# Optimization experiments

Hardware: AMD Instinct MI355X
Metric: run time of the kernel (lower is better)

## Reference

```python
import jax, jax.numpy as jnp
import numpy as np

D_MODEL = 1024
D_STATE = 16
EXPAND = 2
D_CONV = 4
D_INNER = EXPAND * D_MODEL
BATCH = 1
SEQLEN = 2048


def setup_inputs() -> dict:
    key = jax.random.key(0)
    ks = jax.random.split(key, 8)
    s = 0.02
    x = jax.random.normal(ks[0], (BATCH, SEQLEN, D_MODEL), jnp.float32)
    W_in = jax.random.normal(ks[1], (2 * D_INNER, D_MODEL), jnp.float32) * s
    conv_w = jax.random.normal(ks[2], (D_INNER, 1, D_CONV), jnp.float32) * s
    conv_b = jnp.zeros((D_INNER,), jnp.float32)
    # A_log init as in module: log(arange(1, d_state+1)) tiled over d_inner
    A_log = jnp.log(jnp.tile(jnp.arange(1, D_STATE + 1, dtype=jnp.float32), (D_INNER, 1)))
    D_param = jnp.ones((D_INNER,), jnp.float32)
    W_x = jax.random.normal(ks[3], (2 * D_STATE, D_INNER), jnp.float32) * s
    W_dt = jax.random.normal(ks[4], (D_INNER, D_INNER), jnp.float32) * s
    b_dt = jnp.zeros((D_INNER,), jnp.float32)
    W_out = jax.random.normal(ks[5], (D_MODEL, D_INNER), jnp.float32) * s
    return {"x": x, "W_in": W_in, "conv_w": conv_w, "conv_b": conv_b,
            "A_log": A_log, "D_param": D_param, "W_x": W_x,
            "W_dt": W_dt, "b_dt": b_dt, "W_out": W_out}


def reference(x, W_in, conv_w, conv_b, A_log, D_param, W_x, W_dt, b_dt, W_out):
    B_, L, _ = x.shape
    xz = jnp.einsum('bld,ed->ble', x, W_in)          # [B,L,2*d_inner]
    x_inner, z = jnp.split(xz, 2, axis=-1)
    # causal depthwise conv1d (pad left d_conv-1 == torch pad-both + slice[:L])
    xc = jax.lax.conv_general_dilated(
        jnp.swapaxes(x_inner, 1, 2), conv_w, (1,), [(D_CONV - 1, 0)],
        feature_group_count=D_INNER,
        dimension_numbers=('NCH', 'OIH', 'NCH')) + conv_b[None, :, None]
    x_ssm = jnp.swapaxes(jax.nn.silu(xc), 1, 2)       # [B,L,d_inner]
    dt = jax.nn.softplus(jnp.einsum('ble,fe->blf', x_ssm, W_dt) + b_dt)
    x_dbl = jnp.einsum('ble,se->bls', x_ssm, W_x)     # [B,L,2*d_state]
    B_mat, C_mat = jnp.split(x_dbl, 2, axis=-1)       # each [B,L,d_state]
    A = -jnp.exp(A_log)                               # [d_inner,d_state]
    dA = jnp.exp(dt[..., None] * A)                   # [B,L,d_inner,d_state]
    dBx = B_mat[:, :, None, :] * dt[..., None] * x_ssm[..., None]

    def step(h, inp):
        dA_t, dBx_t, C_t = inp
        h = dA_t * h + dBx_t                          # [B,d_inner,d_state]
        y_t = jnp.einsum('bds,bs->bd', h, C_t)
        return h, y_t

    h0 = jnp.zeros((B_, D_INNER, D_STATE), x.dtype)
    _, ys = jax.lax.scan(step, h0, (jnp.swapaxes(dA, 0, 1),
                                    jnp.swapaxes(dBx, 0, 1),
                                    jnp.swapaxes(C_mat, 0, 1)))
    y = jnp.swapaxes(ys, 0, 1) + D_param * x_ssm      # [B,L,d_inner]
    y = y * jax.nn.silu(z)
    out = jnp.einsum('ble,de->bld', y, W_out)
    return out + x
```

## Files before the change

kernel.cpp:

```cpp
#include <hip/hip_runtime.h>

#define L_SEQ 2048
#define DMODEL 1024
#define DINNER 2048
#define NCHUNK 128
#define TCHUNK 16

typedef __attribute__((ext_vector_type(8))) short bf16x8;
typedef __attribute__((ext_vector_type(4))) float f32x4;

__device__ __forceinline__ float bf2f(unsigned short u) {
  return __uint_as_float(((unsigned)u) << 16);
}
__device__ __forceinline__ unsigned short f2bf(float f) {
  unsigned u = __float_as_uint(f);
  return (unsigned short)((u + 0x7FFFu + ((u >> 16) & 1u)) >> 16);
}
__device__ __forceinline__ void gload_lds16(const void* g, void* l) {
  __builtin_amdgcn_global_load_lds(
      (const __attribute__((address_space(1))) void*)g,
      (__attribute__((address_space(3))) void*)l, 16, 0, 0);
}

__global__ void cvt_f32_bf16(const float4* __restrict__ in, ushort4* __restrict__ out, int n4) {
  int i = blockIdx.x * blockDim.x + threadIdx.x;
  if (i >= n4) return;
  float4 v = in[i];
  ushort4 o;
  o.x = f2bf(v.x); o.y = f2bf(v.y); o.z = f2bf(v.z); o.w = f2bf(v.w);
  out[i] = o;
}

__global__ void zero_bf16(ushort4* __restrict__ out, int n4) {
  int i = blockIdx.x * blockDim.x + threadIdx.x;
  if (i >= n4) return;
  out[i] = ushort4{0, 0, 0, 0};
}

template <int EPI>
__global__ __launch_bounds__(256) void gemm_bt3(
    const unsigned short* __restrict__ A, const unsigned short* __restrict__ B,
    int M, int N, int K, int nx, int ksplit,
    float* __restrict__ outf, unsigned short* __restrict__ outb,
    const float* __restrict__ aux) {
  __shared__ __align__(16) unsigned short As[3 * 128 * 32];
  __shared__ __align__(16) unsigned short Bs[3 * 128 * 32];
  const int tid = threadIdx.x;
  const int lane = tid & 63;
  const int wave = tid >> 6;
  const int wm = wave >> 1, wn = wave & 1;

  const int nwg = gridDim.x;
  const int wg = blockIdx.x;
  const int swzb = (wg & 7) * (nwg >> 3) + (wg >> 3);
  const int tiles = nwg / ksplit;
  const int ks = swzb / tiles;
  const int t = swzb - ks * tiles;
  const int bx = t % nx, by = t / nx;
  const int bm = by * 128, bn = bx * 128;
  const int Ks = K / ksplit;
  const int kbeg = ks * Ks;
  const int nk = Ks >> 5;

  const int srow = tid >> 2, sc4 = tid & 3;
  const int scp = sc4 ^ ((srow >> 1) & 3);
  const unsigned short* Ag = A + (size_t)(bm + srow) * K + scp * 8;
  const unsigned short* Bg = B + (size_t)(bn + srow) * K + scp * 8;
  unsigned short* AsW = &As[srow * 32 + sc4 * 8];
  unsigned short* BsW = &Bs[srow * 32 + sc4 * 8];

  auto STAGE = [&](int buf, int k0) {
    gload_lds16(Ag + k0, AsW + buf * 4096);
    gload_lds16(Ag + (size_t)64 * K + k0, AsW + buf * 4096 + 64 * 32);
    gload_lds16(Bg + k0, BsW + buf * 4096);
    gload_lds16(Bg + (size_t)64 * K + k0, BsW + buf * 4096 + 64 * 32);
  };

  f32x4 acc[4][4] = {};

  const int g = lane >> 4;
  const int r16 = lane & 15;
  const int sw = (g ^ ((r16 >> 1) & 3)) * 8;

  STAGE(0, kbeg);
  STAGE(1, kbeg + 32);
  int cur = 0, stg = 2;

  for (int i = 0; i < nk; ++i) {
    if (i < nk - 1) {
      asm volatile("s_waitcnt vmcnt(4)" ::: "memory");
    } else {
      asm volatile("s_waitcnt vmcnt(0)" ::: "memory");
    }
    __builtin_amdgcn_s_barrier();
    asm volatile("" ::: "memory");
    if (i + 2 < nk) {
      STAGE(stg, kbeg + (i + 2) * 32);
      stg = (stg == 2) ? 0 : stg + 1;
    }

    bf16x8 a[4], b[4];
#pragma unroll
    for (int ii = 0; ii < 4; ++ii)
      a[ii] = *(const bf16x8*)&As[cur * 4096 + (wm * 64 + ii * 16 + r16) * 32 + sw];
#pragma unroll
    for (int j = 0; j < 4; ++j)
      b[j] = *(const bf16x8*)&Bs[cur * 4096 + (wn * 64 + j * 16 + r16) * 32 + sw];
#pragma unroll
    for (int ii = 0; ii < 4; ++ii)
#pragma unroll
      for (int j = 0; j < 4; ++j)
        acc[ii][j] = __builtin_amdgcn_mfma_f32_16x16x32_bf16(a[ii], b[j], acc[ii][j], 0, 0, 0);

    cur = (cur == 2) ? 0 : cur + 1;
  }

  const int rq = lane >> 4;
#pragma unroll
  for (int i = 0; i < 4; ++i)
#pragma unroll
    for (int j = 0; j < 4; ++j)
#pragma unroll
      for (int r = 0; r < 4; ++r) {
        int row = bm + wm * 64 + i * 16 + rq * 4 + r;
        int col = bn + wn * 64 + j * 16 + r16;
        float v = acc[i][j][r];
        if (EPI == 0) {
          outb[(size_t)row * N + col] = f2bf(v);
        } else if (EPI == 3) {
          if (col < 2048) {
            float tt = v + aux[col];
            float sp = (tt > 15.f) ? tt : log1pf(__expf(tt));
            outb[(size_t)row * 2048 + col] = f2bf(sp);
          } else if (col < 2080) {
            outf[(size_t)row * 32 + (col - 2048)] = v;
          }
        } else {
          outf[(size_t)ks * M * N + (size_t)row * N + col] = v;
        }
      }
}

__global__ void reduce_addx(const float4* __restrict__ p, const float4* __restrict__ x,
                            float4* __restrict__ out, int n4) {
  int i = blockIdx.x * 256 + threadIdx.x;
  if (i >= n4) return;
  float4 a = p[i], b = p[n4 + i], c = x[i];
  float4 o;
  o.x = a.x + b.x + c.x; o.y = a.y + b.y + c.y;
  o.z = a.z + b.z + c.z; o.w = a.w + b.w + c.w;
  out[i] = o;
}

__global__ __launch_bounds__(256) void conv_silu8(
    const unsigned short* __restrict__ xz,
    const float* __restrict__ cw, const float* __restrict__ cb,
    unsigned short* __restrict__ x_ssm, unsigned short* __restrict__ sz_out) {
  int idx = blockIdx.x * 256 + threadIdx.x;
  int l = idx >> 8, c0 = (idx & 255) * 8;
  float acc[8];
  float4 b0 = *(const float4*)(cb + c0);
  float4 b1 = *(const float4*)(cb + c0 + 4);
  acc[0] = b0.x; acc[1] = b0.y; acc[2] = b0.z; acc[3] = b0.w;
  acc[4] = b1.x; acc[5] = b1.y; acc[6] = b1.z; acc[7] = b1.w;
  float4 w[8];
#pragma unroll
  for (int j = 0; j < 8; ++j) w[j] = *(const float4*)(cw + (c0 + j) * 4);
#pragma unroll
  for (int k = 0; k < 4; ++k) {
    int lt = l - 3 + k;
    if (lt >= 0) {
      bf16x8 v = *(const bf16x8*)(xz + (size_t)lt * 4096 + c0);
      const float* wk = (const float*)w;
#pragma unroll
      for (int j = 0; j < 8; ++j)
        acc[j] = fmaf(bf2f((unsigned short)v[j]), wk[j * 4 + k], acc[j]);
    }
  }
  bf16x8 zr = *(const bf16x8*)(xz + (size_t)l * 4096 + 2048 + c0);
  bf16x8 ox, oz;
#pragma unroll
  for (int j = 0; j < 8; ++j) {
    float a = acc[j];
    ox[j] = (short)f2bf(a / (1.f + __expf(-a)));
    float zv = bf2f((unsigned short)zr[j]);
    oz[j] = (short)f2bf(zv / (1.f + __expf(-zv)));
  }
  *(bf16x8*)(x_ssm + (size_t)idx * 8) = ox;
  *(bf16x8*)(sz_out + (size_t)idx * 8) = oz;
}

__global__ __launch_bounds__(256) void scan_passA(
    const unsigned short* __restrict__ dtb, const unsigned short* __restrict__ x_ssm,
    const float* __restrict__ x_dbl, const float* __restrict__ A_log,
    float* __restrict__ Pout, float* __restrict__ Hout) {
  int tid = threadIdx.x;
  int c = blockIdx.x & (NCHUNK - 1), db = blockIdx.x >> 7;
  int d = db * 256 + tid;
  int t0 = c * TCHUNK;
  float Av[16];
  const float4* al4 = (const float4*)(A_log + d * 16);
#pragma unroll
  for (int q = 0; q < 4; ++q) {
    float4 a = al4[q];
    Av[q * 4 + 0] = -__expf(a.x); Av[q * 4 + 1] = -__expf(a.y);
    Av[q * 4 + 2] = -__expf(a.z); Av[q * 4 + 3] = -__expf(a.w);
  }
  float h[16];
#pragma unroll
  for (int s = 0; s < 16; ++s) h[s] = 0.f;
  float sum_dt = 0.f;
#pragma unroll 2
  for (int i = 0; i < TCHUNK; ++i) {
    int t = t0 + i;
    float dtv = bf2f(dtb[(size_t)t * 2048 + d]);
    float xv = bf2f(x_ssm[(size_t)t * 2048 + d]);
    float dtx = dtv * xv;
    sum_dt += dtv;
    const float* B = x_dbl + t * 32;
#pragma unroll
    for (int s = 0; s < 16; ++s) {
      float dA = __expf(dtv * Av[s]);
      h[s] = fmaf(dA, h[s], B[s] * dtx);
    }
  }
  float* Ho = Hout + (size_t)c * 32768 + d * 16;
  float* Po = Pout + (size_t)c * 32768 + d * 16;
#pragma unroll
  for (int s = 0; s < 16; ++s) Ho[s] = h[s];
#pragma unroll
  for (int s = 0; s < 16; ++s) Po[s] = __expf(sum_dt * Av[s]);
}

__global__ __launch_bounds__(256) void scan_passB(
    float* __restrict__ P, const float* __restrict__ Hloc) {
  int i = blockIdx.x * 256 + threadIdx.x;
  float h = 0.f;
  for (int c = 0; c < NCHUNK; ++c) {
    size_t o = (size_t)c * 32768 + i;
    float p = P[o];
    float hl = Hloc[o];
    P[o] = h;
    h = fmaf(p, h, hl);
  }
}

__global__ __launch_bounds__(256) void scan_passC(
    const unsigned short* __restrict__ dtb, const unsigned short* __restrict__ x_ssm,
    const float* __restrict__ x_dbl, const float* __restrict__ A_log,
    const float* __restrict__ D_param, const unsigned short* __restrict__ silu_z,
    const float* __restrict__ Hinit, unsigned short* __restrict__ y_out) {
  int tid = threadIdx.x;
  int c = blockIdx.x & (NCHUNK - 1), db = blockIdx.x >> 7;
  int d = db * 256 + tid;
  int t0 = c * TCHUNK;
  float Av[16];
  const float4* al4 = (const float4*)(A_log + d * 16);
#pragma unroll
  for (int q = 0; q < 4; ++q) {
    float4 a = al4[q];
    Av[q * 4 + 0] = -__expf(a.x); Av[q * 4 + 1] = -__expf(a.y);
    Av[q * 4 + 2] = -__expf(a.z); Av[q * 4 + 3] = -__expf(a.w);
  }
  float Dp = D_param[d];
  float h[16];
  const float4* hi4 = (const float4*)(Hinit + (size_t)c * 32768 + d * 16);
#pragma unroll
  for (int q = 0; q < 4; ++q) {
    float4 v = hi4[q];
    h[q * 4 + 0] = v.x; h[q * 4 + 1] = v.y; h[q * 4 + 2] = v.z; h[q * 4 + 3] = v.w;
  }
#pragma unroll 2
  for (int i = 0; i < TCHUNK; ++i) {
    int t = t0 + i;
    float dtv = bf2f(dtb[(size_t)t * 2048 + d]);
    float xv = bf2f(x_ssm[(size_t)t * 2048 + d]);
    float dtx = dtv * xv;
    const float* B = x_dbl + t * 32;
    const float* C = x_dbl + t * 32 + 16;
    float y = 0.f;
#pragma unroll
    for (int s = 0; s < 16; ++s) {
      float dA = __expf(dtv * Av[s]);
      h[s] = fmaf(dA, h[s], B[s] * dtx);
      y = fmaf(h[s], C[s], y);
    }
    float szv = bf2f(silu_z[(size_t)t * 2048 + d]);
    y_out[(size_t)t * 2048 + d] = f2bf((y + Dp * xv) * szv);
  }
}

extern "C" void kernel_launch(void* const* d_in, const int* in_sizes, int n_in,
                              void* d_out, int out_size, void* d_ws, size_t ws_size,
                              hipStream_t stream) {
  const float* x      = (const float*)d_in[0];
  const float* W_in   = (const float*)d_in[1];
  const float* conv_w = (const float*)d_in[2];
  const float* conv_b = (const float*)d_in[3];
  const float* A_log  = (const float*)d_in[4];
  const float* D_par  = (const float*)d_in[5];
  const float* W_x    = (const float*)d_in[6];
  const float* W_dt   = (const float*)d_in[7];
  const float* b_dt   = (const float*)d_in[8];
  const float* W_out  = (const float*)d_in[9];
  float* out = (float*)d_out;

  char* ws = (char*)d_ws;
  unsigned short* xbf    = (unsigned short*)(ws + 0);
  unsigned short* Winbf  = (unsigned short*)(ws + ((size_t)4 << 20));
  unsigned short* Wcomb  = (unsigned short*)(ws + ((size_t)12 << 20));
  unsigned short* Woutbf = (unsigned short*)(ws + ((size_t)21 << 20));
  unsigned short* xz     = (unsigned short*)(ws + ((size_t)25 << 20));
  unsigned short* xssm   = (unsigned short*)(ws + ((size_t)41 << 20));
  unsigned short* siluz  = (unsigned short*)(ws + ((size_t)49 << 20));
  unsigned short* dtb    = (unsigned short*)(ws + ((size_t)57 << 20));
  float* xdbl            = (float*)(ws + ((size_t)65 << 20));
  unsigned short* yfin   = (unsigned short*)(ws + ((size_t)66 << 20));
  float* Pbuf            = (float*)(ws + ((size_t)25 << 20));
  float* Hloc            = (float*)(ws + ((size_t)4 << 20));
  float* part            = (float*)(ws + ((size_t)41 << 20));

  cvt_f32_bf16<<<2048, 256, 0, stream>>>((const float4*)x, (ushort4*)xbf, (L_SEQ * DMODEL) / 4);
  cvt_f32_bf16<<<4096, 256, 0, stream>>>((const float4*)W_in, (ushort4*)Winbf, (2 * DINNER * DMODEL) / 4);
  cvt_f32_bf16<<<4096, 256, 0, stream>>>((const float4*)W_dt, (ushort4*)Wcomb, (DINNER * DINNER) / 4);
  cvt_f32_bf16<<<64, 256, 0, stream>>>((const float4*)W_x, (ushort4*)(Wcomb + (size_t)2048 * 2048),
                                       (32 * DINNER) / 4);
  zero_bf16<<<192, 256, 0, stream>>>((ushort4*)(Wcomb + (size_t)2080 * 2048), (96 * DINNER) / 4);
  cvt_f32_bf16<<<2048, 256, 0, stream>>>((const float4*)W_out, (ushort4*)Woutbf, (DMODEL * DINNER) / 4);

  gemm_bt3<0><<<512, 256, 0, stream>>>(xbf, Winbf, L_SEQ, 4096, DMODEL, 32, 1,
                                       nullptr, xz, nullptr);

  conv_silu8<<<2048, 256, 0, stream>>>(xz, conv_w, conv_b, xssm, siluz);

  gemm_bt3<3><<<272, 256, 0, stream>>>(xssm, Wcomb, L_SEQ, 2176, DINNER, 17, 1,
                                       xdbl, dtb, b_dt);

  scan_passA<<<NCHUNK * (DINNER / 256), 256, 0, stream>>>(dtb, xssm, xdbl, A_log, Pbuf, Hloc);
  scan_passB<<<(DINNER * 16) / 256, 256, 0, stream>>>(Pbuf, Hloc);
  scan_passC<<<NCHUNK * (DINNER / 256), 256, 0, stream>>>(dtb, xssm, xdbl, A_log, D_par, siluz,
                                                          Pbuf, yfin);

  gemm_bt3<4><<<256, 256, 0, stream>>>(yfin, Woutbf, L_SEQ, DMODEL, DINNER, 8, 2,
                                       part, nullptr, nullptr);
  reduce_addx<<<(L_SEQ * DMODEL / 4 + 255) / 256, 256, 0, stream>>>(
      (const float4*)part, (const float4*)x, (float4*)out, L_SEQ * DMODEL / 4);
}
```

Baseline: 320.0 us.

## Split-K the dt/out GEMMs with bf16 partials, fuse conversions, halve scan chunks

Merges the six weight/input conversion and zeroing launches into one kernel. Splits the dt/x_dbl GEMM two ways along K and the output GEMM four ways, storing partials in bf16. The softplus epilogue moves into a separate reduction kernel, and the final residual add now sums four partials. The scan now uses 64 chunks of 32 steps instead of 128 of 16, with the workspace layout rearranged. The aim is to raise GEMM occupancy and cut launch and partial-write traffic, at the cost of bf16 rounding on partial sums and extra reduction passes.

New measurement: 277.0 us. 1.16x faster.

```diff
diff --git a/kernel.cpp b/kernel.cpp
--- a/kernel.cpp
+++ b/kernel.cpp
@@ -3,8 +3,8 @@
 #define L_SEQ 2048
 #define DMODEL 1024
 #define DINNER 2048
-#define NCHUNK 128
-#define TCHUNK 16
+#define NCHUNK 64
+#define TCHUNK 32
 
 typedef __attribute__((ext_vector_type(8))) short bf16x8;
 typedef __attribute__((ext_vector_type(4))) float f32x4;
@@ -22,19 +22,24 @@
       (__attribute__((address_space(3))) void*)l, 16, 0, 0);
 }
 
-__global__ void cvt_f32_bf16(const float4* __restrict__ in, ushort4* __restrict__ out, int n4) {
-  int i = blockIdx.x * blockDim.x + threadIdx.x;
-  if (i >= n4) return;
-  float4 v = in[i];
+__global__ __launch_bounds__(256) void cvt_all(
+    const float4* __restrict__ x, const float4* __restrict__ Win,
+    const float4* __restrict__ Wdt, const float4* __restrict__ Wx,
+    const float4* __restrict__ Wout,
+    ushort4* __restrict__ xbf, ushort4* __restrict__ winb, ushort4* __restrict__ wcomb,
+    ushort4* __restrict__ wcombx, ushort4* __restrict__ woutb, ushort4* __restrict__ wcombz) {
+  int i = blockIdx.x * 256 + threadIdx.x;
+  const float4* s; ushort4* d; int j;
+  if (i < 524288)        { s = x;    d = xbf;    j = i; }
+  else if (i < 1572864)  { s = Win;  d = winb;   j = i - 524288; }
+  else if (i < 2621440)  { s = Wdt;  d = wcomb;  j = i - 1572864; }
+  else if (i < 2637824)  { s = Wx;   d = wcombx; j = i - 2621440; }
+  else if (i < 3162112)  { s = Wout; d = woutb;  j = i - 2637824; }
+  else                   { wcombz[i - 3162112] = ushort4{0, 0, 0, 0}; return; }
+  float4 v = s[j];
   ushort4 o;
   o.x = f2bf(v.x); o.y = f2bf(v.y); o.z = f2bf(v.z); o.w = f2bf(v.w);
-  out[i] = o;
-}
-
-__global__ void zero_bf16(ushort4* __restrict__ out, int n4) {
-  int i = blockIdx.x * blockDim.x + threadIdx.x;
-  if (i >= n4) return;
-  out[i] = ushort4{0, 0, 0, 0};
+  d[j] = o;
 }
 
 template <int EPI>
@@ -127,29 +132,66 @@
         float v = acc[i][j][r];
         if (EPI == 0) {
           outb[(size_t)row * N + col] = f2bf(v);
-        } else if (EPI == 3) {
-          if (col < 2048) {
-            float tt = v + aux[col];
-            float sp = (tt > 15.f) ? tt : log1pf(__expf(tt));
-            outb[(size_t)row * 2048 + col] = f2bf(sp);
-          } else if (col < 2080) {
-            outf[(size_t)row * 32 + (col - 2048)] = v;
-          }
         } else {
-          outf[(size_t)ks * M * N + (size_t)row * N + col] = v;
+          outb[(size_t)ks * M * N + (size_t)row * N + col] = f2bf(v);
         }
       }
 }
 
-__global__ void reduce_addx(const float4* __restrict__ p, const float4* __restrict__ x,
-                            float4* __restrict__ out, int n4) {
+__global__ __launch_bounds__(256) void g2reduce(
+    const unsigned short* __restrict__ p, const float* __restrict__ bdt,
+    unsigned short* __restrict__ dtb, float* __restrict__ xdbl) {
+  int b = blockIdx.x;
+  if (b < 2048) {
+    int c0 = threadIdx.x * 8;
+    size_t o0 = (size_t)b * 2176 + c0;
+    bf16x8 v0 = *(const bf16x8*)(p + o0);
+    bf16x8 v1 = *(const bf16x8*)(p + (size_t)2048 * 2176 + o0);
+    float4 ba = *(const float4*)(bdt + c0);
+    float4 bb = *(const float4*)(bdt + c0 + 4);
+    float bv[8] = {ba.x, ba.y, ba.z, ba.w, bb.x, bb.y, bb.z, bb.w};
+    bf16x8 o;
+#pragma unroll
+    for (int j = 0; j < 8; ++j) {
+      float t = bf2f((unsigned short)v0[j]) + bf2f((unsigned short)v1[j]) + bv[j];
+      float sp = (t > 15.f) ? t : log1pf(__expf(t));
+      o[j] = (short)f2bf(sp);
+    }
+    *(bf16x8*)(dtb + (size_t)b * 2048 + c0) = o;
+  } else {
+    int idx = (b - 2048) * 256 + threadIdx.x;
+    int row = idx >> 3, c4 = (idx & 7) * 4;
+    size_t o0 = (size_t)row * 2176 + 2048 + c4;
+    float4 r;
+    r.x = bf2f(p[o0 + 0]) + bf2f(p[(size_t)2048 * 2176 + o0 + 0]);
+    r.y = bf2f(p[o0 + 1]) + bf2f(p[(size_t)2048 * 2176 + o0 + 1]);
+    r.z = bf2f(p[o0 + 2]) + bf2f(p[(size_t)2048 * 2176 + o0 + 2]);
+    r.w = bf2f(p[o0 + 3]) + bf2f(p[(size_t)2048 * 2176 + o0 + 3]);
+    *(float4*)(xdbl + row * 32 + c4) = r;
+  }
+}
+
+__global__ __launch_bounds__(256) void addx4(
+    const unsigned short* __restrict__ p, const float* __restrict__ x,
+    float* __restrict__ out) {
   int i = blockIdx.x * 256 + threadIdx.x;
-  if (i >= n4) return;
-  float4 a = p[i], b = p[n4 + i], c = x[i];
-  float4 o;
-  o.x = a.x + b.x + c.x; o.y = a.y + b.y + c.y;
-  o.z = a.z + b.z + c.z; o.w = a.w + b.w + c.w;
-  out[i] = o;
+  size_t base = (size_t)i * 8;
+  bf16x8 a0 = *(const bf16x8*)(p + base);
+  bf16x8 a1 = *(const bf16x8*)(p + 2097152 + base);
+  bf16x8 a2 = *(const bf16x8*)(p + 4194304 + base);
+  bf16x8 a3 = *(const bf16x8*)(p + 6291456 + base);
+  float4 x0 = *(const float4*)(x + base);
+  float4 x1 = *(const float4*)(x + base + 4);
+  float xs[8] = {x0.x, x0.y, x0.z, x0.w, x1.x, x1.y, x1.z, x1.w};
+  float4 o0, o1;
+#pragma unroll
+  for (int j = 0; j < 8; ++j) {
+    float v = bf2f((unsigned short)a0[j]) + bf2f((unsigned short)a1[j]) +
+              bf2f((unsigned short)a2[j]) + bf2f((unsigned short)a3[j]) + xs[j];
+    if (j < 4) ((float*)&o0)[j] = v; else ((float*)&o1)[j - 4] = v;
+  }
+  *(float4*)(out + base) = o0;
+  *(float4*)(out + base + 4) = o1;
 }
 
 __global__ __launch_bounds__(256) void conv_silu8(
@@ -195,7 +237,7 @@
     const float* __restrict__ x_dbl, const float* __restrict__ A_log,
     float* __restrict__ Pout, float* __restrict__ Hout) {
   int tid = threadIdx.x;
-  int c = blockIdx.x & (NCHUNK - 1), db = blockIdx.x >> 7;
+  int c = blockIdx.x & (NCHUNK - 1), db = blockIdx.x / NCHUNK;
   int d = db * 256 + tid;
   int t0 = c * TCHUNK;
   float Av[16];
@@ -236,6 +278,7 @@
     float* __restrict__ P, const float* __restrict__ Hloc) {
   int i = blockIdx.x * 256 + threadIdx.x;
   float h = 0.f;
+#pragma unroll 8
   for (int c = 0; c < NCHUNK; ++c) {
     size_t o = (size_t)c * 32768 + i;
     float p = P[o];
@@ -251,7 +294,7 @@
     const float* __restrict__ D_param, const unsigned short* __restrict__ silu_z,
     const float* __restrict__ Hinit, unsigned short* __restrict__ y_out) {
   int tid = threadIdx.x;
-  int c = blockIdx.x & (NCHUNK - 1), db = blockIdx.x >> 7;
+  int c = blockIdx.x & (NCHUNK - 1), db = blockIdx.x / NCHUNK;
   int d = db * 256 + tid;
   int t0 = c * TCHUNK;
   float Av[16];
@@ -309,40 +352,40 @@
   unsigned short* xbf    = (unsigned short*)(ws + 0);
   unsigned short* Winbf  = (unsigned short*)(ws + ((size_t)4 << 20));
   unsigned short* Wcomb  = (unsigned short*)(ws + ((size_t)12 << 20));
+  float* xdbl            = (float*)(ws + ((size_t)41 << 19));
   unsigned short* Woutbf = (unsigned short*)(ws + ((size_t)21 << 20));
   unsigned short* xz     = (unsigned short*)(ws + ((size_t)25 << 20));
-  unsigned short* xssm   = (unsigned short*)(ws + ((size_t)41 << 20));
-  unsigned short* siluz  = (unsigned short*)(ws + ((size_t)49 << 20));
-  unsigned short* dtb    = (unsigned short*)(ws + ((size_t)57 << 20));
-  float* xdbl            = (float*)(ws + ((size_t)65 << 20));
-  unsigned short* yfin   = (unsigned short*)(ws + ((size_t)66 << 20));
-  float* Pbuf            = (float*)(ws + ((size_t)25 << 20));
-  float* Hloc            = (float*)(ws + ((size_t)4 << 20));
-  float* part            = (float*)(ws + ((size_t)41 << 20));
-
-  cvt_f32_bf16<<<2048, 256, 0, stream>>>((const float4*)x, (ushort4*)xbf, (L_SEQ * DMODEL) / 4);
-  cvt_f32_bf16<<<4096, 256, 0, stream>>>((const float4*)W_in, (ushort4*)Winbf, (2 * DINNER * DMODEL) / 4);
-  cvt_f32_bf16<<<4096, 256, 0, stream>>>((const float4*)W_dt, (ushort4*)Wcomb, (DINNER * DINNER) / 4);
-  cvt_f32_bf16<<<64, 256, 0, stream>>>((const float4*)W_x, (ushort4*)(Wcomb + (size_t)2048 * 2048),
-                                       (32 * DINNER) / 4);
-  zero_bf16<<<192, 256, 0, stream>>>((ushort4*)(Wcomb + (size_t)2080 * 2048), (96 * DINNER) / 4);
-  cvt_f32_bf16<<<2048, 256, 0, stream>>>((const float4*)W_out, (ushort4*)Woutbf, (DMODEL * DINNER) / 4);
+  unsigned short* part2  = (unsigned short*)(ws + ((size_t)25 << 20));
+  unsigned short* yfin   = (unsigned short*)(ws + ((size_t)25 << 20));
+  unsigned short* part4  = (unsigned short*)(ws + ((size_t)33 << 20));
+  unsigned short* xssm   = (unsigned short*)(ws + ((size_t)50 << 20));
+  unsigned short* siluz  = (unsigned short*)(ws + ((size_t)58 << 20));
+  unsigned short* dtb    = (unsigned short*)(ws + ((size_t)66 << 20));
+  float* Pbuf            = (float*)(ws + 0);
+  float* Hloc            = (float*)(ws + ((size_t)12 << 20));
+
+  cvt_all<<<12544, 256, 0, stream>>>(
+      (const float4*)x, (const float4*)W_in, (const float4*)W_dt, (const float4*)W_x,
+      (const float4*)W_out,
+      (ushort4*)xbf, (ushort4*)Winbf, (ushort4*)Wcomb,
+      (ushort4*)(Wcomb + (size_t)2048 * 2048), (ushort4*)Woutbf,
+      (ushort4*)(Wcomb + (size_t)2080 * 2048));
 
   gemm_bt3<0><<<512, 256, 0, stream>>>(xbf, Winbf, L_SEQ, 4096, DMODEL, 32, 1,
                                        nullptr, xz, nullptr);
 
   conv_silu8<<<2048, 256, 0, stream>>>(xz, conv_w, conv_b, xssm, siluz);
 
-  gemm_bt3<3><<<272, 256, 0, stream>>>(xssm, Wcomb, L_SEQ, 2176, DINNER, 17, 1,
-                                       xdbl, dtb, b_dt);
+  gemm_bt3<5><<<544, 256, 0, stream>>>(xssm, Wcomb, L_SEQ, 2176, DINNER, 17, 2,
+                                       nullptr, part2, nullptr);
+  g2reduce<<<2048 + 64, 256, 0, stream>>>(part2, b_dt, dtb, xdbl);
 
   scan_passA<<<NCHUNK * (DINNER / 256), 256, 0, stream>>>(dtb, xssm, xdbl, A_log, Pbuf, Hloc);
   scan_passB<<<(DINNER * 16) / 256, 256, 0, stream>>>(Pbuf, Hloc);
   scan_passC<<<NCHUNK * (DINNER / 256), 256, 0, stream>>>(dtb, xssm, xdbl, A_log, D_par, siluz,
                                                           Pbuf, yfin);
 
-  gemm_bt3<4><<<256, 256, 0, stream>>>(yfin, Woutbf, L_SEQ, DMODEL, DINNER, 8, 2,
-                                       part, nullptr, nullptr);
-  reduce_addx<<<(L_SEQ * DMODEL / 4 + 255) / 256, 256, 0, stream>>>(
-      (const float4*)part, (const float4*)x, (float4*)out, L_SEQ * DMODEL / 4);
-}
+  gemm_bt3<5><<<512, 256, 0, stream>>>(yfin, Woutbf, L_SEQ, DMODEL, DINNER, 8, 4,
+                                       nullptr, part4, nullptr);
+  addx4<<<1024, 256, 0, stream>>>(part4, x, out);
+}
```

## Templatize GEMM tile sizes, fuse conversions, drop split-K, and halve scan chunks

Applied to the files above, without the earlier changes.

Merges all fp32-to-bf16 weight/input conversions and the zero fill into one kernel launch. Templatizes the GEMM on tile shape and uses smaller 64x128 and 64x64 tiles, so the grids grow to 1024, 544 and 512 blocks. The out-projection drops split-K and the separate reduce kernel by adding the residual in the GEMM epilogue. The scan now uses 64 chunks of 32 steps instead of 128 of 16, and its buffers are moved to separate workspace regions. Smaller tiles improve occupancy and CU coverage but lower data reuse per tile, and the longer chunks cut parallelism in the scan passes.

After: 297.6 us. 7.0% less time.

```diff
diff --git a/kernel.cpp b/kernel.cpp
--- a/kernel.cpp
+++ b/kernel.cpp
@@ -3,8 +3,8 @@
 #define L_SEQ 2048
 #define DMODEL 1024
 #define DINNER 2048
-#define NCHUNK 128
-#define TCHUNK 16
+#define NCHUNK 64
+#define TCHUNK 32
 
 typedef __attribute__((ext_vector_type(8))) short bf16x8;
 typedef __attribute__((ext_vector_type(4))) float f32x4;
@@ -22,29 +22,36 @@
       (__attribute__((address_space(3))) void*)l, 16, 0, 0);
 }
 
-__global__ void cvt_f32_bf16(const float4* __restrict__ in, ushort4* __restrict__ out, int n4) {
-  int i = blockIdx.x * blockDim.x + threadIdx.x;
-  if (i >= n4) return;
-  float4 v = in[i];
+__global__ __launch_bounds__(256) void cvt_all(
+    const float4* __restrict__ x, const float4* __restrict__ Win,
+    const float4* __restrict__ Wdt, const float4* __restrict__ Wx,
+    const float4* __restrict__ Wout,
+    ushort4* __restrict__ xbf, ushort4* __restrict__ winb, ushort4* __restrict__ wcomb,
+    ushort4* __restrict__ wcombx, ushort4* __restrict__ woutb, ushort4* __restrict__ wcombz) {
+  int i = blockIdx.x * 256 + threadIdx.x;
+  const float4* s; ushort4* d; int j;
+  if (i < 524288)        { s = x;    d = xbf;    j = i; }
+  else if (i < 1572864)  { s = Win;  d = winb;   j = i - 524288; }
+  else if (i < 2621440)  { s = Wdt;  d = wcomb;  j = i - 1572864; }
+  else if (i < 2637824)  { s = Wx;   d = wcombx; j = i - 2621440; }
+  else if (i < 3162112)  { s = Wout; d = woutb;  j = i - 2637824; }
+  else                   { wcombz[i - 3162112] = ushort4{0, 0, 0, 0}; return; }
+  float4 v = s[j];
   ushort4 o;
   o.x = f2bf(v.x); o.y = f2bf(v.y); o.z = f2bf(v.z); o.w = f2bf(v.w);
-  out[i] = o;
-}
-
-__global__ void zero_bf16(ushort4* __restrict__ out, int n4) {
-  int i = blockIdx.x * blockDim.x + threadIdx.x;
-  if (i >= n4) return;
-  out[i] = ushort4{0, 0, 0, 0};
-}
-
-template <int EPI>
-__global__ __launch_bounds__(256) void gemm_bt3(
+  d[j] = o;
+}
+
+template <int MI, int NJ, int EPI>
+__global__ __launch_bounds__(256) void gemm_t(
     const unsigned short* __restrict__ A, const unsigned short* __restrict__ B,
-    int M, int N, int K, int nx, int ksplit,
+    int M, int N, int K, int nx,
     float* __restrict__ outf, unsigned short* __restrict__ outb,
-    const float* __restrict__ aux) {
-  __shared__ __align__(16) unsigned short As[3 * 128 * 32];
-  __shared__ __align__(16) unsigned short Bs[3 * 128 * 32];
+    const float* __restrict__ aux, const float* __restrict__ resid) {
+  constexpr int BM = MI * 32, BN = NJ * 32;
+  constexpr int SA = MI / 2, SB = NJ / 2, S = SA + SB;
+  __shared__ __align__(16) unsigned short As[3 * BM * 32];
+  __shared__ __align__(16) unsigned short Bs[3 * BN * 32];
   const int tid = threadIdx.x;
   const int lane = tid & 63;
   const int wave = tid >> 6;
@@ -53,14 +60,9 @@
   const int nwg = gridDim.x;
   const int wg = blockIdx.x;
   const int swzb = (wg & 7) * (nwg >> 3) + (wg >> 3);
-  const int tiles = nwg / ksplit;
-  const int ks = swzb / tiles;
-  const int t = swzb - ks * tiles;
-  const int bx = t % nx, by = t / nx;
-  const int bm = by * 128, bn = bx * 128;
-  const int Ks = K / ksplit;
-  const int kbeg = ks * Ks;
-  const int nk = Ks >> 5;
+  const int bx = swzb % nx, by = swzb / nx;
+  const int bm = by * BM, bn = bx * BN;
+  const int nk = K >> 5;
 
   const int srow = tid >> 2, sc4 = tid & 3;
   const int scp = sc4 ^ ((srow >> 1) & 3);
@@ -70,46 +72,50 @@
   unsigned short* BsW = &Bs[srow * 32 + sc4 * 8];
 
   auto STAGE = [&](int buf, int k0) {
-    gload_lds16(Ag + k0, AsW + buf * 4096);
-    gload_lds16(Ag + (size_t)64 * K + k0, AsW + buf * 4096 + 64 * 32);
-    gload_lds16(Bg + k0, BsW + buf * 4096);
-    gload_lds16(Bg + (size_t)64 * K + k0, BsW + buf * 4096 + 64 * 32);
+#pragma unroll
+    for (int q = 0; q < SA; ++q)
+      gload_lds16(Ag + (size_t)q * 64 * K + k0, AsW + buf * BM * 32 + q * 64 * 32);
+#pragma unroll
+    for (int q = 0; q < SB; ++q)
+      gload_lds16(Bg + (size_t)q * 64 * K + k0, BsW + buf * BN * 32 + q * 64 * 32);
   };
 
-  f32x4 acc[4][4] = {};
+  f32x4 acc[MI][NJ] = {};
 
   const int g = lane >> 4;
   const int r16 = lane & 15;
   const int sw = (g ^ ((r16 >> 1) & 3)) * 8;
 
-  STAGE(0, kbeg);
-  STAGE(1, kbeg + 32);
+  STAGE(0, 0);
+  STAGE(1, 32);
   int cur = 0, stg = 2;
 
   for (int i = 0; i < nk; ++i) {
     if (i < nk - 1) {
-      asm volatile("s_waitcnt vmcnt(4)" ::: "memory");
+      if constexpr (S == 2) asm volatile("s_waitcnt vmcnt(2)" ::: "memory");
+      else if constexpr (S == 3) asm volatile("s_waitcnt vmcnt(3)" ::: "memory");
+      else asm volatile("s_waitcnt vmcnt(4)" ::: "memory");
     } else {
       asm volatile("s_waitcnt vmcnt(0)" ::: "memory");
     }
     __builtin_amdgcn_s_barrier();
     asm volatile("" ::: "memory");
     if (i + 2 < nk) {
-      STAGE(stg, kbeg + (i + 2) * 32);
+      STAGE(stg, (i + 2) * 32);
       stg = (stg == 2) ? 0 : stg + 1;
     }
 
-    bf16x8 a[4], b[4];
-#pragma unroll
-    for (int ii = 0; ii < 4; ++ii)
-      a[ii] = *(const bf16x8*)&As[cur * 4096 + (wm * 64 + ii * 16 + r16) * 32 + sw];
-#pragma unroll
-    for (int j = 0; j < 4; ++j)
-      b[j] = *(const bf16x8*)&Bs[cur * 4096 + (wn * 64 + j * 16 + r16) * 32 + sw];
-#pragma unroll
-    for (int ii = 0; ii < 4; ++ii)
-#pragma unroll
-      for (int j = 0; j < 4; ++j)
+    bf16x8 a[MI], b[NJ];
+#pragma unroll
+    for (int ii = 0; ii < MI; ++ii)
+      a[ii] = *(const bf16x8*)&As[cur * BM * 32 + (wm * MI * 16 + ii * 16 + r16) * 32 + sw];
+#pragma unroll
+    for (int j = 0; j < NJ; ++j)
+      b[j] = *(const bf16x8*)&Bs[cur * BN * 32 + (wn * NJ * 16 + j * 16 + r16) * 32 + sw];
+#pragma unroll
+    for (int ii = 0; ii < MI; ++ii)
+#pragma unroll
+      for (int j = 0; j < NJ; ++j)
         acc[ii][j] = __builtin_amdgcn_mfma_f32_16x16x32_bf16(a[ii], b[j], acc[ii][j], 0, 0, 0);
 
     cur = (cur == 2) ? 0 : cur + 1;
@@ -117,39 +123,29 @@
 
   const int rq = lane >> 4;
 #pragma unroll
-  for (int i = 0; i < 4; ++i)
-#pragma unroll
-    for (int j = 0; j < 4; ++j)
+  for (int i = 0; i < MI; ++i)
+#pragma unroll
+    for (int j = 0; j < NJ; ++j)
 #pragma unroll
       for (int r = 0; r < 4; ++r) {
-        int row = bm + wm * 64 + i * 16 + rq * 4 + r;
-        int col = bn + wn * 64 + j * 16 + r16;
+        int row = bm + wm * MI * 16 + i * 16 + rq * 4 + r;
+        int col = bn + wn * NJ * 16 + j * 16 + r16;
         float v = acc[i][j][r];
         if (EPI == 0) {
           outb[(size_t)row * N + col] = f2bf(v);
-        } else if (EPI == 3) {
+        } else if (EPI == 2) {
+          size_t off = (size_t)row * N + col;
+          outf[off] = v + resid[off];
+        } else {
           if (col < 2048) {
-            float tt = v + aux[col];
-            float sp = (tt > 15.f) ? tt : log1pf(__expf(tt));
+            float t = v + aux[col];
+            float sp = (t > 15.f) ? t : log1pf(__expf(t));
             outb[(size_t)row * 2048 + col] = f2bf(sp);
           } else if (col < 2080) {
             outf[(size_t)row * 32 + (col - 2048)] = v;
           }
-        } else {
-          outf[(size_t)ks * M * N + (size_t)row * N + col] = v;
         }
       }
-}
-
-__global__ void reduce_addx(const float4* __restrict__ p, const float4* __restrict__ x,
-                            float4* __restrict__ out, int n4) {
-  int i = blockIdx.x * 256 + threadIdx.x;
-  if (i >= n4) return;
-  float4 a = p[i], b = p[n4 + i], c = x[i];
-  float4 o;
-  o.x = a.x + b.x + c.x; o.y = a.y + b.y + c.y;
-  o.z = a.z + b.z + c.z; o.w = a.w + b.w + c.w;
-  out[i] = o;
 }
 
 __global__ __launch_bounds__(256) void conv_silu8(
@@ -195,7 +191,7 @@
     const float* __restrict__ x_dbl, const float* __restrict__ A_log,
     float* __restrict__ Pout, float* __restrict__ Hout) {
   int tid = threadIdx.x;
-  int c = blockIdx.x & (NCHUNK - 1), db = blockIdx.x >> 7;
+  int c = blockIdx.x & (NCHUNK - 1), db = blockIdx.x / NCHUNK;
   int d = db * 256 + tid;
   int t0 = c * TCHUNK;
   float Av[16];
@@ -236,6 +232,7 @@
     float* __restrict__ P, const float* __restrict__ Hloc) {
   int i = blockIdx.x * 256 + threadIdx.x;
   float h = 0.f;
+#pragma unroll 8
   for (int c = 0; c < NCHUNK; ++c) {
     size_t o = (size_t)c * 32768 + i;
     float p = P[o];
@@ -251,7 +248,7 @@
     const float* __restrict__ D_param, const unsigned short* __restrict__ silu_z,
     const float* __restrict__ Hinit, unsigned short* __restrict__ y_out) {
   int tid = threadIdx.x;
-  int c = blockIdx.x & (NCHUNK - 1), db = blockIdx.x >> 7;
+  int c = blockIdx.x & (NCHUNK - 1), db = blockIdx.x / NCHUNK;
   int d = db * 256 + tid;
   int t0 = c * TCHUNK;
   float Av[16];
@@ -316,33 +313,29 @@
   unsigned short* dtb    = (unsigned short*)(ws + ((size_t)57 << 20));
   float* xdbl            = (float*)(ws + ((size_t)65 << 20));
   unsigned short* yfin   = (unsigned short*)(ws + ((size_t)66 << 20));
-  float* Pbuf            = (float*)(ws + ((size_t)25 << 20));
-  float* Hloc            = (float*)(ws + ((size_t)4 << 20));
-  float* part            = (float*)(ws + ((size_t)41 << 20));
-
-  cvt_f32_bf16<<<2048, 256, 0, stream>>>((const float4*)x, (ushort4*)xbf, (L_SEQ * DMODEL) / 4);
-  cvt_f32_bf16<<<4096, 256, 0, stream>>>((const float4*)W_in, (ushort4*)Winbf, (2 * DINNER * DMODEL) / 4);
-  cvt_f32_bf16<<<4096, 256, 0, stream>>>((const float4*)W_dt, (ushort4*)Wcomb, (DINNER * DINNER) / 4);
-  cvt_f32_bf16<<<64, 256, 0, stream>>>((const float4*)W_x, (ushort4*)(Wcomb + (size_t)2048 * 2048),
-                                       (32 * DINNER) / 4);
-  zero_bf16<<<192, 256, 0, stream>>>((ushort4*)(Wcomb + (size_t)2080 * 2048), (96 * DINNER) / 4);
-  cvt_f32_bf16<<<2048, 256, 0, stream>>>((const float4*)W_out, (ushort4*)Woutbf, (DMODEL * DINNER) / 4);
-
-  gemm_bt3<0><<<512, 256, 0, stream>>>(xbf, Winbf, L_SEQ, 4096, DMODEL, 32, 1,
-                                       nullptr, xz, nullptr);
+  float* Pbuf            = (float*)(ws + ((size_t)74 << 20));
+  float* Hloc            = (float*)(ws + ((size_t)82 << 20));
+
+  cvt_all<<<12544, 256, 0, stream>>>(
+      (const float4*)x, (const float4*)W_in, (const float4*)W_dt, (const float4*)W_x,
+      (const float4*)W_out,
+      (ushort4*)xbf, (ushort4*)Winbf, (ushort4*)Wcomb,
+      (ushort4*)(Wcomb + (size_t)2048 * 2048), (ushort4*)Woutbf,
+      (ushort4*)(Wcomb + (size_t)2080 * 2048));
+
+  gemm_t<2, 4, 0><<<1024, 256, 0, stream>>>(xbf, Winbf, L_SEQ, 4096, DMODEL, 32,
+                                            nullptr, xz, nullptr, nullptr);
 
   conv_silu8<<<2048, 256, 0, stream>>>(xz, conv_w, conv_b, xssm, siluz);
 
-  gemm_bt3<3><<<272, 256, 0, stream>>>(xssm, Wcomb, L_SEQ, 2176, DINNER, 17, 1,
-                                       xdbl, dtb, b_dt);
+  gemm_t<2, 4, 3><<<544, 256, 0, stream>>>(xssm, Wcomb, L_SEQ, 2176, DINNER, 17,
+                                           xdbl, dtb, b_dt, nullptr);
 
   scan_passA<<<NCHUNK * (DINNER / 256), 256, 0, stream>>>(dtb, xssm, xdbl, A_log, Pbuf, Hloc);
   scan_passB<<<(DINNER * 16) / 256, 256, 0, stream>>>(Pbuf, Hloc);
   scan_passC<<<NCHUNK * (DINNER / 256), 256, 0, stream>>>(dtb, xssm, xdbl, A_log, D_par, siluz,
                                                           Pbuf, yfin);
 
-  gemm_bt3<4><<<256, 256, 0, stream>>>(yfin, Woutbf, L_SEQ, DMODEL, DINNER, 8, 2,
-                                       part, nullptr, nullptr);
-  reduce_addx<<<(L_SEQ * DMODEL / 4 + 255) / 256, 256, 0, stream>>>(
-      (const float4*)part, (const float4*)x, (float4*)out, L_SEQ * DMODEL / 4);
-}
+  gemm_t<2, 2, 2><<<512, 256, 0, stream>>>(yfin, Woutbf, L_SEQ, DMODEL, DINNER, 16,
+                                           out, nullptr, nullptr, x);
+}
```
